# Kernel tuning notes

Measured on AMD Instinct MI355X. Metric: run time of the kernel, lower is better.

The kernel has to match this reference:

```python
import jax, jax.numpy as jnp
import numpy as np

D_BINS = 16   # piecewise-linear bins
N_PROP = 10   # hard-coded in CountModule.__init__


def pwl(w, x):
    """PiecewiseLinear.forward: w is [D_BINS+1], x any shape in [0,1]."""
    aw = jnp.abs(w)
    nw = aw / aw.sum()
    cs = jnp.cumsum(nw)               # [17] cumulative knot values
    xd = x * D_BINS
    ip = jnp.floor(xd).astype(jnp.int32)   # x >= 0 so trunc == floor
    frac = xd - ip.astype(x.dtype)
    return cs[jnp.minimum(ip, D_BINS)] + frac * nw[jnp.minimum(ip + 1, D_BINS)]


def iou(a):
    """Pairwise IoU of boxes a [B,4,n] (coords y1,x1,y2,x2) -> [B,n,n]."""
    tl = jnp.maximum(a[:, :2, :, None], a[:, :2, None, :])  # [B,2,n,n]
    br = jnp.minimum(a[:, 2:, :, None], a[:, 2:, None, :])
    wh = jnp.clip(br - tl, 0.0)
    inter = wh[:, 0] * wh[:, 1]                               # [B,n,n]
    area = jnp.clip(a[:, 2] - a[:, 0], 0.0) * jnp.clip(a[:, 3] - a[:, 1], 0.0)  # [B,n]
    return inter / (area[:, :, None] + area[:, None, :] - inter + 1e-12)


def count_forward(boxes, attention, f_weights):
    n = N_PROP
    B = boxes.shape[0]
    f = lambda i, x: pwl(f_weights[i], x)
    # keep top-n proposals by attention score
    att_v, idx = jax.lax.top_k(attention, n)                  # [B,n]
    boxes_f = jnp.take_along_axis(
        boxes, jnp.broadcast_to(idx[:, None, :], (B, 4, n)), axis=2)  # [B,4,n]
    att = jax.nn.sigmoid(att_v)
    A = att[:, :, None] * att[:, None, :]                     # outer product [B,n,n]
    Dm = 1.0 - iou(boxes_f)                                   # [B,n,n]
    A_t = f(0, A) * f(1, Dm)
    X = f(3, A) * f(4, Dm)
    # deduplicate: outer_diff on 2D att gives pairwise |a_i - a_j|; on 3D X the
    # original torch code unsqueezes both operands at the same axis, yielding zeros
    att_diff = jnp.abs(att[:, :, None] - att[:, None, :])     # [B,n,n]
    xs = X[:, :, None, :]
    score_diff = jnp.broadcast_to(jnp.abs(xs - xs), (B, n, n, n))  # zeros, as in torch
    sim = f(2, 1.0 - att_diff) * jnp.prod(f(2, 1.0 - score_diff), axis=1)  # [B,n,n]
    s_i = sim.sum(axis=2)                                     # [B,n]
    s_st = s_i[:, :, None] * s_i[:, None, :]                  # [B,n,n]
    score = A_t / s_st
    corr = f(0, att * att) / s_i
    mod_E = score.sum(axis=(1, 2))[:, None] + corr.sum(axis=1, keepdims=True)  # [B,1]
    c = jnp.sqrt(mod_E + 1e-20)
    # to_k_hot: soft two-hot over counts 0..n
    cc = jnp.clip(c, 0.0, float(n))                           # [B,1]
    ip = jnp.floor(cc).astype(jnp.int32)
    frac = cc - ip.astype(cc.dtype)
    left = jax.nn.one_hot(jnp.minimum(ip[:, 0], n), n + 1, dtype=cc.dtype)
    right = jax.nn.one_hot(jnp.minimum(ip[:, 0] + 1, n), n + 1, dtype=cc.dtype)
    o = (1.0 - frac) * left + frac * right                    # [B,n+1]
    p_a = jnp.abs(f(5, att) - 0.5)                            # [B,n]
    p_d = jnp.abs(f(6, Dm) - 0.5)                             # [B,n,n]
    gate = f(7, p_a.mean(axis=1, keepdims=True)
             + p_d.mean(axis=2).mean(axis=1, keepdims=True))  # [B,1]
    return gate * o                                           # [B,n+1]


def setup_inputs() -> dict:
    key = jax.random.key(0)
    k1, k2, k3 = jax.random.split(key, 3)
    B, M = 32768, 36
    boxes = jax.random.uniform(k1, (B, 4, M), dtype=jnp.float32)
    attention = jax.random.normal(k2, (B, M), dtype=jnp.float32)
    f_weights = jax.random.uniform(k3, (8, D_BINS + 1), dtype=jnp.float32,
                                   minval=0.25, maxval=1.75)
    return {"boxes": boxes, "attention": attention, "f_weights": f_weights}


def reference(boxes, attention, f_weights):
    return count_forward(boxes, attention, f_weights)
```

## Files before the change

kernel.cpp:

```cpp
#include <hip/hip_runtime.h>
#include <cstdint>
#include <cstddef>

#define MM 36
#define NP 10
#define BLOCK 256

__device__ __forceinline__ float pwl_eval(const float2* __restrict__ Trow, float x) {
    float xd = x * 16.0f;
    float fip = floorf(xd);
    float frac = xd - fip;
    int ip = (int)fip;
    ip = ip < 0 ? 0 : (ip > 16 ? 16 : ip);
    float2 t = Trow[ip];
    return t.x + frac * t.y;
}

__device__ __forceinline__ unsigned long long umax64(unsigned long long a, unsigned long long b) {
    return a > b ? a : b;
}

__device__ __forceinline__ unsigned long long pack_key(float v, int m) {
    unsigned u = __float_as_uint(v);
    u = ((int)u < 0) ? ~u : (u | 0x80000000u);
    return ((unsigned long long)u << 32) | (unsigned)(63 - m);
}

__global__ __launch_bounds__(BLOCK, 4) void count_kernel(
    const float* __restrict__ boxes,
    const float* __restrict__ attention,
    const float* __restrict__ fw,
    float* __restrict__ out,
    int B)
{
    __shared__ float2 T[8][17];

    const int tid = threadIdx.x;

    if (tid < 8) {
        const float* w = fw + tid * 17;
        float aw[17];
        float s = 0.f;
        #pragma unroll
        for (int k = 0; k < 17; ++k) { aw[k] = fabsf(w[k]); s += aw[k]; }
        float nw[17];
        #pragma unroll
        for (int k = 0; k < 17; ++k) nw[k] = aw[k] / s;
        float c = 0.f;
        #pragma unroll
        for (int k = 0; k < 17; ++k) {
            c += nw[k];
            T[tid][k] = make_float2(c, (k < 16) ? nw[k + 1] : nw[16]);
        }
    }
    __syncthreads();

    const int lane = tid & 63;
    const int l    = lane & 15;
    const int b    = blockIdx.x * (BLOCK / 16) + (tid >> 4);
    if (b >= B) return;

    const float* arow = attention + (size_t)b * MM;
    const float* brow = boxes + (size_t)b * (4 * MM);

    unsigned long long k0 = pack_key(arow[l], l);
    unsigned long long k1 = pack_key(arow[l + 16], l + 16);
    unsigned long long k2 = (l < 4) ? pack_key(arow[l + 32], l + 32) : 0ull;

    unsigned long long packed = 0ull;
    #pragma unroll
    for (int t = 0; t < NP; ++t) {
        unsigned long long km = umax64(umax64(k0, k1), k2);
        km = umax64(km, __shfl_xor(km, 1));
        km = umax64(km, __shfl_xor(km, 2));
        km = umax64(km, __shfl_xor(km, 4));
        km = umax64(km, __shfl_xor(km, 8));
        int mt = 63 - (int)(km & 63ull);
        packed |= ((unsigned long long)mt) << (6 * t);
        k0 = (mt == l)      ? 0ull : k0;
        k1 = (mt == l + 16) ? 0ull : k1;
        k2 = (mt == l + 32) ? 0ull : k2;
    }

    float satt[NP], y1[NP], x1[NP], y2[NP], x2[NP], area[NP], at[NP];
    #pragma unroll
    for (int t = 0; t < NP; ++t) {
        int m = (int)((packed >> (6 * t)) & 63ull);
        float av = arow[m];
        satt[t] = 1.0f / (1.0f + __expf(-av));
        float a0 = brow[m];
        float a1 = brow[m + MM];
        float a2 = brow[m + 2 * MM];
        float a3 = brow[m + 3 * MM];
        y1[t] = a0; x1[t] = a1; y2[t] = a2; x2[t] = a3;
        area[t] = fmaxf(a2 - a0, 0.f) * fmaxf(a3 - a1, 0.f);
        at[t] = 0.f;
    }

    float cs2_16 = T[2][16].x;
    float p2 = cs2_16 * cs2_16;
    float p4 = p2 * p2;
    float p8 = p4 * p4;
    float P = p8 * p2;

    const float2* T0 = &T[0][0];
    const float2* T1 = &T[1][0];
    const float2* T2 = &T[2][0];
    const float2* T5 = &T[5][0];
    const float2* T6 = &T[6][0];
    const float2* T7 = &T[7][0];

    float s_i = 0.f, pd_i = 0.f, pa_i = 0.f;
    float sattI = 0.f;
    if (l < NP) {
        int mo = (int)((packed >> (6 * l)) & 63ull);
        float av = arow[mo];
        sattI = 1.0f / (1.0f + __expf(-av));
        float y1I = brow[mo];
        float x1I = brow[mo + MM];
        float y2I = brow[mo + 2 * MM];
        float x2I = brow[mo + 3 * MM];
        float areaI = fmaxf(y2I - y1I, 0.f) * fmaxf(x2I - x1I, 0.f);

        #pragma unroll
        for (int j = 0; j < NP; ++j) {
            float ty = fmaxf(y1I, y1[j]);
            float tx = fmaxf(x1I, x1[j]);
            float by = fminf(y2I, y2[j]);
            float bx = fminf(x2I, x2[j]);
            float ih = fmaxf(by - ty, 0.f);
            float iw = fmaxf(bx - tx, 0.f);
            float inter = ih * iw;
            float iouv = __fdividef(inter, areaI + area[j] - inter + 1e-12f);
            float Dm = fmaxf(1.0f - iouv, 0.0f);
            float A = sattI * satt[j];
            at[j] = pwl_eval(T0, A) * pwl_eval(T1, Dm);
            s_i += pwl_eval(T2, 1.0f - fabsf(sattI - satt[j])) * P;
            pd_i += fabsf(pwl_eval(T6, Dm) - 0.5f);
        }
        pa_i = fabsf(pwl_eval(T5, sattI) - 0.5f);
    }

    float inv_i = 1.0f / s_i;
    const int gbase = lane & 48;
    float dot = 0.f;
    #pragma unroll
    for (int j = 0; j < NP; ++j) {
        float ivj = __shfl(inv_i, gbase + j);
        dot = fmaf(at[j], ivj, dot);
    }
    float score_i = inv_i * dot;
    float corr_i = pwl_eval(T0, sattI * sattI) * inv_i;
    float contrib = (l < NP) ? (score_i + corr_i) : 0.f;

    #pragma unroll
    for (int s = 1; s < 16; s <<= 1) {
        contrib += __shfl_xor(contrib, s);
        pa_i    += __shfl_xor(pa_i, s);
        pd_i    += __shfl_xor(pd_i, s);
    }

    float gate = pwl_eval(T7, pa_i * 0.1f + pd_i * 0.01f);
    float cval = sqrtf(contrib + 1e-20f);
    cval = fminf(fmaxf(cval, 0.f), 10.0f);
    float fip = floorf(cval);
    int ipc = (int)fip;
    float frac = cval - fip;
    int i0 = ipc < 10 ? ipc : 10;
    int i1 = (ipc + 1) < 10 ? (ipc + 1) : 10;

    if (l < NP + 1) {
        float val = ((l == i0) ? (1.0f - frac) * gate : 0.f)
                  + ((l == i1) ? frac * gate : 0.f);
        out[(size_t)b * (NP + 1) + l] = val;
    }
}

extern "C" void kernel_launch(void* const* d_in, const int* in_sizes, int n_in,
                              void* d_out, int out_size, void* d_ws, size_t ws_size,
                              hipStream_t stream) {
    const float* boxes = (const float*)d_in[0];
    const float* attention = (const float*)d_in[1];
    const float* fw = (const float*)d_in[2];
    float* out = (float*)d_out;
    int B = in_sizes[1] / MM;
    int batches_per_block = BLOCK / 16;
    int grid = (B + batches_per_block - 1) / batches_per_block;
    hipLaunchKernelGGL(count_kernel, dim3(grid), dim3(BLOCK), 0, stream,
                       boxes, attention, fw, out, B);
}
```

Measured before the change: 28.73 us.

## Rework top-k selection with DPP max+ballot and share proposals via LDS

The top-10 selection now uses a 32-bit float row max built from DPP moves plus ballots to find the winning index, replacing 64-bit packed-key shuffle reductions. Each lane loads only its own gathered proposal and publishes it to shared memory, instead of every lane gathering all ten boxes from global memory. The inverse similarity sums are shared through LDS rather than shuffles, and the per-group reductions use DPP row sums. The early return becomes a clamped batch index with a masked store, so all lanes reach the barrier. The shared-memory exchange relies on lanes of the same wavefront running in lockstep, with no extra barrier between the write and the read.

```diff
diff --git a/kernel.cpp b/kernel.cpp
--- a/kernel.cpp
+++ b/kernel.cpp
@@ -5,6 +5,27 @@
 #define MM 36
 #define NP 10
 #define BLOCK 256
+#define GPB (BLOCK / 16)
+
+template<int CTRL>
+__device__ __forceinline__ float dpp_movf(float x) {
+    return __int_as_float(__builtin_amdgcn_update_dpp(
+        0, __float_as_int(x), CTRL, 0xF, 0xF, true));
+}
+__device__ __forceinline__ float rowmax16(float x) {
+    x = fmaxf(x, dpp_movf<0xB1>(x));
+    x = fmaxf(x, dpp_movf<0x4E>(x));
+    x = fmaxf(x, dpp_movf<0x141>(x));
+    x = fmaxf(x, dpp_movf<0x140>(x));
+    return x;
+}
+__device__ __forceinline__ float rowsum16(float x) {
+    x += dpp_movf<0xB1>(x);
+    x += dpp_movf<0x4E>(x);
+    x += dpp_movf<0x141>(x);
+    x += dpp_movf<0x140>(x);
+    return x;
+}
 
 __device__ __forceinline__ float pwl_eval(const float2* __restrict__ Trow, float x) {
     float xd = x * 16.0f;
@@ -16,17 +37,7 @@
     return t.x + frac * t.y;
 }
 
-__device__ __forceinline__ unsigned long long umax64(unsigned long long a, unsigned long long b) {
-    return a > b ? a : b;
-}
-
-__device__ __forceinline__ unsigned long long pack_key(float v, int m) {
-    unsigned u = __float_as_uint(v);
-    u = ((int)u < 0) ? ~u : (u | 0x80000000u);
-    return ((unsigned long long)u << 32) | (unsigned)(63 - m);
-}
-
-__global__ __launch_bounds__(BLOCK, 4) void count_kernel(
+__global__ __launch_bounds__(BLOCK) void count_kernel(
     const float* __restrict__ boxes,
     const float* __restrict__ attention,
     const float* __restrict__ fw,
@@ -34,6 +45,8 @@
     int B)
 {
     __shared__ float2 T[8][17];
+    __shared__ float2 prop[GPB][NP][3];
+    __shared__ __align__(8) float invl[GPB][NP];
 
     const int tid = threadIdx.x;
 
@@ -53,48 +66,56 @@
             T[tid][k] = make_float2(c, (k < 16) ? nw[k + 1] : nw[16]);
         }
     }
-    __syncthreads();
 
     const int lane = tid & 63;
-    const int l    = lane & 15;
-    const int b    = blockIdx.x * (BLOCK / 16) + (tid >> 4);
-    if (b >= B) return;
+    const int l    = tid & 15;
+    const int g    = tid >> 4;
+    int b = blockIdx.x * GPB + g;
+    const bool valid = (b < B);
+    b = valid ? b : (B - 1);
 
     const float* arow = attention + (size_t)b * MM;
     const float* brow = boxes + (size_t)b * (4 * MM);
 
-    unsigned long long k0 = pack_key(arow[l], l);
-    unsigned long long k1 = pack_key(arow[l + 16], l + 16);
-    unsigned long long k2 = (l < 4) ? pack_key(arow[l + 32], l + 32) : 0ull;
+    float v0 = arow[l];
+    float v1 = arow[l + 16];
+    float v2 = (l < 4) ? arow[l + 32] : -INFINITY;
+
+    __syncthreads();
 
     unsigned long long packed = 0ull;
+    const int gbase = lane & 48;
     #pragma unroll
     for (int t = 0; t < NP; ++t) {
-        unsigned long long km = umax64(umax64(k0, k1), k2);
-        km = umax64(km, __shfl_xor(km, 1));
-        km = umax64(km, __shfl_xor(km, 2));
-        km = umax64(km, __shfl_xor(km, 4));
-        km = umax64(km, __shfl_xor(km, 8));
-        int mt = 63 - (int)(km & 63ull);
-        packed |= ((unsigned long long)mt) << (6 * t);
-        k0 = (mt == l)      ? 0ull : k0;
-        k1 = (mt == l + 16) ? 0ull : k1;
-        k2 = (mt == l + 32) ? 0ull : k2;
-    }
-
-    float satt[NP], y1[NP], x1[NP], y2[NP], x2[NP], area[NP], at[NP];
-    #pragma unroll
-    for (int t = 0; t < NP; ++t) {
-        int m = (int)((packed >> (6 * t)) & 63ull);
-        float av = arow[m];
-        satt[t] = 1.0f / (1.0f + __expf(-av));
-        float a0 = brow[m];
-        float a1 = brow[m + MM];
-        float a2 = brow[m + 2 * MM];
-        float a3 = brow[m + 3 * MM];
-        y1[t] = a0; x1[t] = a1; y2[t] = a2; x2[t] = a3;
-        area[t] = fmaxf(a2 - a0, 0.f) * fmaxf(a3 - a1, 0.f);
-        at[t] = 0.f;
+        float vm = rowmax16(fmaxf(fmaxf(v0, v1), v2));
+        unsigned long long b0 = __ballot(v0 == vm);
+        unsigned long long b1 = __ballot(v1 == vm);
+        unsigned long long b2 = __ballot(v2 == vm);
+        unsigned g0 = (unsigned)((b0 >> gbase) & 0xFFFFull);
+        unsigned g1 = (unsigned)((b1 >> gbase) & 0xFFFFull);
+        unsigned g2 = (unsigned)((b2 >> gbase) & 0xFFFFull);
+        int m = g0 ? (__ffs(g0) - 1)
+              : (g1 ? (__ffs(g1) + 15)
+                    : (__ffs(g2) + 31));
+        packed |= ((unsigned long long)m) << (6 * t);
+        v0 = (m == l)      ? -INFINITY : v0;
+        v1 = (m == l + 16) ? -INFINITY : v1;
+        v2 = (m == l + 32) ? -INFINITY : v2;
+    }
+
+    float sattI = 0.f, y1I = 0.f, x1I = 0.f, y2I = 0.f, x2I = 0.f, areaI = 0.f;
+    if (l < NP) {
+        int mo = (int)((packed >> (6 * l)) & 63ull);
+        float av = arow[mo];
+        sattI = 1.0f / (1.0f + __expf(-av));
+        y1I = brow[mo];
+        x1I = brow[mo + MM];
+        y2I = brow[mo + 2 * MM];
+        x2I = brow[mo + 3 * MM];
+        areaI = fmaxf(y2I - y1I, 0.f) * fmaxf(x2I - x1I, 0.f);
+        prop[g][l][0] = make_float2(y1I, x1I);
+        prop[g][l][1] = make_float2(y2I, x2I);
+        prop[g][l][2] = make_float2(areaI, sattI);
     }
 
     float cs2_16 = T[2][16].x;
@@ -110,57 +131,49 @@
     const float2* T6 = &T[6][0];
     const float2* T7 = &T[7][0];
 
-    float s_i = 0.f, pd_i = 0.f, pa_i = 0.f;
-    float sattI = 0.f;
-    if (l < NP) {
-        int mo = (int)((packed >> (6 * l)) & 63ull);
-        float av = arow[mo];
-        sattI = 1.0f / (1.0f + __expf(-av));
-        float y1I = brow[mo];
-        float x1I = brow[mo + MM];
-        float y2I = brow[mo + 2 * MM];
-        float x2I = brow[mo + 3 * MM];
-        float areaI = fmaxf(y2I - y1I, 0.f) * fmaxf(x2I - x1I, 0.f);
-
-        #pragma unroll
-        for (int j = 0; j < NP; ++j) {
-            float ty = fmaxf(y1I, y1[j]);
-            float tx = fmaxf(x1I, x1[j]);
-            float by = fminf(y2I, y2[j]);
-            float bx = fminf(x2I, x2[j]);
-            float ih = fmaxf(by - ty, 0.f);
-            float iw = fmaxf(bx - tx, 0.f);
-            float inter = ih * iw;
-            float iouv = __fdividef(inter, areaI + area[j] - inter + 1e-12f);
-            float Dm = fmaxf(1.0f - iouv, 0.0f);
-            float A = sattI * satt[j];
-            at[j] = pwl_eval(T0, A) * pwl_eval(T1, Dm);
-            s_i += pwl_eval(T2, 1.0f - fabsf(sattI - satt[j])) * P;
-            pd_i += fabsf(pwl_eval(T6, Dm) - 0.5f);
-        }
-        pa_i = fabsf(pwl_eval(T5, sattI) - 0.5f);
-    }
-
-    float inv_i = 1.0f / s_i;
-    const int gbase = lane & 48;
-    float dot = 0.f;
+    float at[NP];
+    float s_i = 0.f, pdAcc = 0.f;
     #pragma unroll
     for (int j = 0; j < NP; ++j) {
-        float ivj = __shfl(inv_i, gbase + j);
-        dot = fmaf(at[j], ivj, dot);
-    }
-    float score_i = inv_i * dot;
-    float corr_i = pwl_eval(T0, sattI * sattI) * inv_i;
-    float contrib = (l < NP) ? (score_i + corr_i) : 0.f;
-
+        float2 p0 = prop[g][j][0];
+        float2 p1 = prop[g][j][1];
+        float2 p2v = prop[g][j][2];
+        float ty = fmaxf(y1I, p0.x);
+        float tx = fmaxf(x1I, p0.y);
+        float by = fminf(y2I, p1.x);
+        float bx = fminf(x2I, p1.y);
+        float inter = fmaxf(by - ty, 0.f) * fmaxf(bx - tx, 0.f);
+        float iouv = __fdividef(inter, areaI + p2v.x - inter + 1e-12f);
+        float Dm = fmaxf(1.0f - iouv, 0.0f);
+        float A = sattI * p2v.y;
+        at[j] = pwl_eval(T0, A) * pwl_eval(T1, Dm);
+        s_i += pwl_eval(T2, 1.0f - fabsf(sattI - p2v.y)) * P;
+        pdAcc += fabsf(pwl_eval(T6, Dm) - 0.5f);
+    }
+
+    float inv_i = 1.0f / s_i;
+    if (l < NP) invl[g][l] = inv_i;
+
+    float dot = 0.f;
+    const float2* ivp = reinterpret_cast<const float2*>(&invl[g][0]);
     #pragma unroll
-    for (int s = 1; s < 16; s <<= 1) {
-        contrib += __shfl_xor(contrib, s);
-        pa_i    += __shfl_xor(pa_i, s);
-        pd_i    += __shfl_xor(pd_i, s);
-    }
-
-    float gate = pwl_eval(T7, pa_i * 0.1f + pd_i * 0.01f);
+    for (int jj = 0; jj < NP / 2; ++jj) {
+        float2 iv = ivp[jj];
+        dot = fmaf(at[2 * jj], iv.x, dot);
+        dot = fmaf(at[2 * jj + 1], iv.y, dot);
+    }
+
+    float corr = pwl_eval(T0, sattI * sattI) * inv_i;
+    float fmask = (l < NP) ? 1.f : 0.f;
+    float contrib = fmask * (inv_i * dot + corr);
+    float pav = fmask * fabsf(pwl_eval(T5, sattI) - 0.5f);
+    float pdv = fmask * pdAcc;
+
+    contrib = rowsum16(contrib);
+    pav = rowsum16(pav);
+    pdv = rowsum16(pdv);
+
+    float gate = pwl_eval(T7, pav * 0.1f + pdv * 0.01f);
     float cval = sqrtf(contrib + 1e-20f);
     cval = fminf(fmaxf(cval, 0.f), 10.0f);
     float fip = floorf(cval);
@@ -169,7 +182,7 @@
     int i0 = ipc < 10 ? ipc : 10;
     int i1 = (ipc + 1) < 10 ? (ipc + 1) : 10;
 
-    if (l < NP + 1) {
+    if (valid && l < NP + 1) {
         float val = ((l == i0) ? (1.0f - frac) * gate : 0.f)
                   + ((l == i1) ? frac * gate : 0.f);
         out[(size_t)b * (NP + 1) + l] = val;
@@ -184,8 +197,7 @@
     const float* fw = (const float*)d_in[2];
     float* out = (float*)d_out;
     int B = in_sizes[1] / MM;
-    int batches_per_block = BLOCK / 16;
-    int grid = (B + batches_per_block - 1) / batches_per_block;
+    int grid = (B + GPB - 1) / GPB;
     hipLaunchKernelGGL(count_kernel, dim3(grid), dim3(BLOCK), 0, stream,
                        boxes, attention, fw, out, B);
 }
```

Measured after the change: 24.64 us. 14.2% less time.
